# Kernel optimization log

Hardware: AMD Instinct MI355X
Metric: run time of the kernel (lower is better)

The kernel has to match this reference:

```python
import jax, jax.numpy as jnp
import numpy as np

B, S, D = 4, 2048, 1024

def setup_inputs() -> dict:
    key = jax.random.key(0)
    ks = jax.random.split(key, 9)
    q = jax.random.normal(ks[0], (B, S, D), dtype=jnp.float32)
    k = jax.random.normal(ks[1], (B, S, D), dtype=jnp.float32)
    v = jax.random.normal(ks[2], (B, S, D), dtype=jnp.float32)
    # Dense layer params (Glorot-ish scale), bias included like keras Dense
    sc = 1.0 / np.sqrt(D)
    Wq = jax.random.normal(ks[3], (D, D), dtype=jnp.float32) * sc
    Wk = jax.random.normal(ks[4], (D, D), dtype=jnp.float32) * sc
    Wv = jax.random.normal(ks[5], (D, D), dtype=jnp.float32) * sc
    bq = jnp.zeros((D,), dtype=jnp.float32)
    bk = jnp.zeros((D,), dtype=jnp.float32)
    bv = jnp.zeros((D,), dtype=jnp.float32)
    # causal mask: 1 where attention is forbidden (future positions)
    mask = jnp.triu(jnp.ones((S, S), dtype=jnp.float32), k=1)
    return {"q": q, "k": k, "v": v, "mask": mask,
            "Wq": Wq, "bq": bq, "Wk": Wk, "bk": bk, "Wv": Wv, "bv": bv}

def reference(q, k, v, mask, Wq, bq, Wk, bk, Wv, bv):
    WQ = q @ Wq + bq                      # [B,S,D]
    WK = k @ Wk + bk
    WV = v @ Wv + bv
    d_k = jnp.asarray(WK.shape[-1], dtype=jnp.float32)
    scores = jnp.einsum('bqd,bkd->bqk', WQ, WK) / jnp.sqrt(d_k)  # [B,S,S]
    scores = scores + mask * (-1e9)
    attn = jax.nn.softmax(scores, axis=-1)
    return jnp.einsum('bqk,bkd->bqd', attn, WV)
```

## Files before the change

kernel.cpp:

```cpp
#include <hip/hip_runtime.h>
#include <math.h>

#define S_LEN 2048
#define D_DIM 1024
#define NB    4

typedef __bf16 bf16_t;
typedef __bf16 bf16x8 __attribute__((ext_vector_type(8)));
typedef float  f32x4  __attribute__((ext_vector_type(4)));
typedef unsigned int   u32;
typedef unsigned short u16;
typedef unsigned int   u32x4 __attribute__((ext_vector_type(4)));

#define BM 128
#define BN 128
#define BK 64

__device__ __forceinline__ u16 f2b_bits(float x) {
    bf16_t h = (bf16_t)x;
    return *(u16*)&h;
}

__device__ __forceinline__ void async16(const void* g, void* l) {
    __builtin_amdgcn_global_load_lds(
        (__attribute__((address_space(1))) const void*)g,
        (__attribute__((address_space(3))) void*)l, 16, 0, 0);
}

#define BAR_RAW() asm volatile("s_barrier" ::: "memory")

__device__ __forceinline__ void gemm_bt_core(
    const bf16_t* __restrict__ A, const bf16_t* __restrict__ Bt,
    int lda, int ldb, int m0, int n0, int kTiles, f32x4 (&acc)[4][4])
{
    __shared__ bf16_t lA[BM * BK];
    __shared__ bf16_t lB[BN * BK];
    const int t    = threadIdx.x;
    const int w    = t >> 6;
    const int lane = t & 63;
    const int wr   = w >> 1, wc = w & 1;
    const int srow   = lane >> 3;
    const int kb_src = ((lane & 7) ^ (lane >> 3)) * 8;
    const int fr = lane & 15, fq = lane >> 4;
    const int fof0 = (((0 * 4 + fq) ^ (fr & 7)) * 8);
    const int fof1 = (((1 * 4 + fq) ^ (fr & 7)) * 8);
    const bf16_t* paB0 = lA + (wr * 64 + fr) * BK + fof0;
    const bf16_t* paB1 = lA + (wr * 64 + fr) * BK + fof1;
    const bf16_t* pbB0 = lB + (wc * 64 + fr) * BK + fof0;
    const bf16_t* pbB1 = lB + (wc * 64 + fr) * BK + fof1;
    bf16_t* ldsA = lA + (w * 32) * BK;
    bf16_t* ldsB = lB + (w * 32) * BK;
    const bf16_t* gA = A  + (long)(m0 + w * 32 + srow) * lda + kb_src;
    const bf16_t* gB = Bt + (long)(n0 + w * 32 + srow) * ldb + kb_src;

#pragma unroll
    for (int mt = 0; mt < 4; ++mt)
#pragma unroll
        for (int nt = 0; nt < 4; ++nt)
            acc[mt][nt] = f32x4{0.f, 0.f, 0.f, 0.f};

    for (int kt = 0; kt < kTiles; ++kt) {
        const long k0 = (long)kt * BK;
#pragma unroll
        for (int i = 0; i < 4; ++i) {
            async16(gA + k0 + (long)(i * 8) * lda, ldsA + i * 8 * BK);
            async16(gB + k0 + (long)(i * 8) * ldb, ldsB + i * 8 * BK);
        }
        asm volatile("s_waitcnt vmcnt(0)" ::: "memory");
        __syncthreads();
#pragma unroll
        for (int h = 0; h < 2; ++h) {
            const bf16_t* pa = h ? paB1 : paB0;
            const bf16_t* pb = h ? pbB1 : pbB0;
            bf16x8 af[4], bfv[4];
#pragma unroll
            for (int mt = 0; mt < 4; ++mt)
                af[mt] = *(const bf16x8*)(pa + mt * 16 * BK);
#pragma unroll
            for (int nt = 0; nt < 4; ++nt)
                bfv[nt] = *(const bf16x8*)(pb + nt * 16 * BK);
#pragma unroll
            for (int mt = 0; mt < 4; ++mt)
#pragma unroll
                for (int nt = 0; nt < 4; ++nt)
                    acc[mt][nt] = __builtin_amdgcn_mfma_f32_16x16x32_bf16(
                        af[mt], bfv[nt], acc[mt][nt], 0, 0, 0);
        }
        __syncthreads();
    }
}

__device__ __forceinline__ void gemm_bt_dbuf(
    const bf16_t* __restrict__ A, const bf16_t* __restrict__ Bt,
    int lda, int ldb, int m0, int n0, int kTiles, f32x4 (&acc)[4][4])
{
    __shared__ bf16_t lA[2][BM * BK];
    __shared__ bf16_t lB[2][BN * BK];
    const int t    = threadIdx.x;
    const int w    = t >> 6;
    const int lane = t & 63;
    const int wr   = w >> 1, wc = w & 1;
    const int srow   = lane >> 3;
    const int kb_src = ((lane & 7) ^ (lane >> 3)) * 8;
    const int fr = lane & 15, fq = lane >> 4;
    const int fof0 = (((0 * 4 + fq) ^ (fr & 7)) * 8);
    const int fof1 = (((1 * 4 + fq) ^ (fr & 7)) * 8);
    const int aO0 = (wr * 64 + fr) * BK + fof0;
    const int aO1 = (wr * 64 + fr) * BK + fof1;
    const int bO0 = (wc * 64 + fr) * BK + fof0;
    const int bO1 = (wc * 64 + fr) * BK + fof1;
    const int sOf = (w * 32) * BK;
    const bf16_t* gA = A  + (long)(m0 + w * 32 + srow) * lda + kb_src;
    const bf16_t* gB = Bt + (long)(n0 + w * 32 + srow) * ldb + kb_src;

#pragma unroll
    for (int mt = 0; mt < 4; ++mt)
#pragma unroll
        for (int nt = 0; nt < 4; ++nt)
            acc[mt][nt] = f32x4{0.f, 0.f, 0.f, 0.f};

#pragma unroll
    for (int i = 0; i < 4; ++i) {
        async16(gA + (long)(i * 8) * lda, &lA[0][sOf + i * 8 * BK]);
        async16(gB + (long)(i * 8) * ldb, &lB[0][sOf + i * 8 * BK]);
    }

    for (int kt = 0; kt < kTiles; ++kt) {
        const int cur = kt & 1, nxt = cur ^ 1;
        if (kt + 1 < kTiles) {
            const long k1 = (long)(kt + 1) * BK;
#pragma unroll
            for (int i = 0; i < 4; ++i) {
                async16(gA + k1 + (long)(i * 8) * lda, &lA[nxt][sOf + i * 8 * BK]);
                async16(gB + k1 + (long)(i * 8) * ldb, &lB[nxt][sOf + i * 8 * BK]);
            }
            asm volatile("s_waitcnt vmcnt(8)" ::: "memory");
        } else {
            asm volatile("s_waitcnt vmcnt(0)" ::: "memory");
        }
        BAR_RAW();
        const bf16_t* lac = lA[cur];
        const bf16_t* lbc = lB[cur];
#pragma unroll
        for (int h = 0; h < 2; ++h) {
            const bf16_t* pa = lac + (h ? aO1 : aO0);
            const bf16_t* pb = lbc + (h ? bO1 : bO0);
            bf16x8 af[4], bfv[4];
#pragma unroll
            for (int mt = 0; mt < 4; ++mt)
                af[mt] = *(const bf16x8*)(pa + mt * 16 * BK);
#pragma unroll
            for (int nt = 0; nt < 4; ++nt)
                bfv[nt] = *(const bf16x8*)(pb + nt * 16 * BK);
#pragma unroll
            for (int mt = 0; mt < 4; ++mt)
#pragma unroll
                for (int nt = 0; nt < 4; ++nt)
                    acc[mt][nt] = __builtin_amdgcn_mfma_f32_16x16x32_bf16(
                        af[mt], bfv[nt], acc[mt][nt], 0, 0, 0);
        }
        BAR_RAW();
    }
}

__global__ __launch_bounds__(256) void k_f2b(
    const float* __restrict__ q, const float* __restrict__ k,
    const float* __restrict__ v, bf16_t* __restrict__ Xb)
{
    const int z = blockIdx.z;
    const float* src = (z == 0) ? q : ((z == 1) ? k : v);
    bf16_t* dst = Xb + (long)z * ((long)NB * S_LEN * D_DIM);
    const long i = (long)blockIdx.x * blockDim.x + threadIdx.x;
    float4 a = ((const float4*)src)[i];
    u32 lo = (u32)f2b_bits(a.x) | ((u32)f2b_bits(a.y) << 16);
    u32 hi = (u32)f2b_bits(a.z) | ((u32)f2b_bits(a.w) << 16);
    ((uint2*)(dst))[i] = make_uint2(lo, hi);
}

__global__ __launch_bounds__(256) void k_tw(
    const float* __restrict__ Wq, const float* __restrict__ Wk,
    const float* __restrict__ Wv, bf16_t* __restrict__ Wt)
{
    __shared__ u32 tile[64][33];
    const int z = blockIdx.z;
    const float* W = (z == 0) ? Wq : ((z == 1) ? Wk : Wv);
    bf16_t* T = Wt + (long)z * D_DIM * D_DIM;
    const int t = threadIdx.x;
    const int k0 = blockIdx.x * 64, n0 = blockIdx.y * 64;
#pragma unroll
    for (int rr = 0; rr < 4; ++rr) {
        const int kr = (t >> 4) + rr * 16;
        const int nq = (t & 15) * 4;
        float4 f = *(const float4*)(W + (long)(k0 + kr) * D_DIM + n0 + nq);
        tile[kr][(nq >> 1)]     = (u32)f2b_bits(f.x) | ((u32)f2b_bits(f.y) << 16);
        tile[kr][(nq >> 1) + 1] = (u32)f2b_bits(f.z) | ((u32)f2b_bits(f.w) << 16);
    }
    __syncthreads();
#pragma unroll
    for (int rr = 0; rr < 2; ++rr) {
        const int nr = (t >> 3) + rr * 32;
        const int j0 = (t & 7) * 4;
        u32x4 o;
#pragma unroll
        for (int jj = 0; jj < 4; ++jj) {
            const int j = j0 + jj;
            const u32 ua = tile[2 * j][nr >> 1];
            const u32 ub = tile[2 * j + 1][nr >> 1];
            const u32 lo = (nr & 1) ? (ua >> 16) : (ua & 0xffffu);
            const u32 hi = (nr & 1) ? (ub >> 16) : (ub & 0xffffu);
            o[jj] = lo | (hi << 16);
        }
        *(u32x4*)(T + (long)(n0 + nr) * D_DIM + k0 + 2 * j0) = o;
    }
}

__global__ __launch_bounds__(256) void k_tv(
    const bf16_t* __restrict__ PrV, bf16_t* __restrict__ WVt)
{
    __shared__ u32 tile[64][33];
    const int b = blockIdx.z;
    const bf16_t* src = PrV + (long)b * S_LEN * D_DIM;
    bf16_t* dst = WVt + (long)b * D_DIM * S_LEN;
    const int t = threadIdx.x;
    const int d0 = blockIdx.x * 64, s0 = blockIdx.y * 64;
#pragma unroll
    for (int rr = 0; rr < 2; ++rr) {
        const int sr = (t >> 3) + rr * 32;
        const int dp0 = (t & 7) * 4;
        u32x4 u = *(const u32x4*)(src + (long)(s0 + sr) * D_DIM + d0 + 2 * dp0);
#pragma unroll
        for (int q = 0; q < 4; ++q) tile[sr][dp0 + q] = u[q];
    }
    __syncthreads();
#pragma unroll
    for (int rr = 0; rr < 2; ++rr) {
        const int dr = (t >> 3) + rr * 32;
        const int j0 = (t & 7) * 4;
        u32x4 o;
#pragma unroll
        for (int jj = 0; jj < 4; ++jj) {
            const int j = j0 + jj;
            const u32 ua = tile[2 * j][dr >> 1];
            const u32 ub = tile[2 * j + 1][dr >> 1];
            const u32 lo = (dr & 1) ? (ua >> 16) : (ua & 0xffffu);
            const u32 hi = (dr & 1) ? (ub >> 16) : (ub & 0xffffu);
            o[jj] = lo | (hi << 16);
        }
        *(u32x4*)(dst + (long)(d0 + dr) * S_LEN + s0 + 2 * j0) = o;
    }
}

__global__ __launch_bounds__(256) void k_gemm_proj(
    const bf16_t* __restrict__ Xb, const bf16_t* __restrict__ Wt,
    const float* __restrict__ bq, const float* __restrict__ bk,
    const float* __restrict__ bv, bf16_t* __restrict__ Pr)
{
    const int z = blockIdx.z;
    const bf16_t* A  = Xb + (long)z * ((long)NB * S_LEN * D_DIM);
    const bf16_t* Bt = Wt + (long)z * D_DIM * D_DIM;
    bf16_t* C        = Pr + (long)z * ((long)NB * S_LEN * D_DIM);
    const float* bias = (z == 0) ? bq : ((z == 1) ? bk : bv);
    const int m0 = blockIdx.x * BM, n0 = blockIdx.y * BN;
    f32x4 acc[4][4];
    gemm_bt_core(A, Bt, D_DIM, D_DIM, m0, n0, D_DIM / BK, acc);
    const int lane = threadIdx.x & 63, w = threadIdx.x >> 6;
    const int wr = w >> 1, wc = w & 1;
    const int r0 = m0 + wr * 64 + (lane >> 4) * 4;
    const int c0 = n0 + wc * 64 + (lane & 15);
#pragma unroll
    for (int mt = 0; mt < 4; ++mt)
#pragma unroll
        for (int nt = 0; nt < 4; ++nt) {
            const int col = c0 + nt * 16;
            const float bb = bias[col];
#pragma unroll
            for (int r = 0; r < 4; ++r) {
                const int row = r0 + mt * 16 + r;
                C[(long)row * D_DIM + col] = (bf16_t)(acc[mt][nt][r] + bb);
            }
        }
}

__global__ __launch_bounds__(256) void k_gemm_scores(
    const bf16_t* __restrict__ PrQ, const bf16_t* __restrict__ PrK,
    bf16_t* __restrict__ SC)
{
    const int u = blockIdx.x, b = blockIdx.z;
    int ti = (int)((sqrtf(8.0f * (float)u + 1.0f) - 1.0f) * 0.5f);
    while ((ti + 1) * (ti + 2) / 2 <= u) ++ti;
    while (ti * (ti + 1) / 2 > u) --ti;
    const int tj = u - ti * (ti + 1) / 2;
    const bf16_t* A  = PrQ + (long)b * S_LEN * D_DIM;
    const bf16_t* Bt = PrK + (long)b * S_LEN * D_DIM;
    bf16_t* C        = SC  + (long)b * S_LEN * S_LEN;
    const int m0 = ti * BM, n0 = tj * BN;
    f32x4 acc[4][4];
    gemm_bt_dbuf(A, Bt, D_DIM, D_DIM, m0, n0, D_DIM / BK, acc);
    const int lane = threadIdx.x & 63, w = threadIdx.x >> 6;
    const int wr = w >> 1, wc = w & 1;
    const int r0 = m0 + wr * 64 + (lane >> 4) * 4;
    const int c0 = n0 + wc * 64 + (lane & 15);
#pragma unroll
    for (int mt = 0; mt < 4; ++mt)
#pragma unroll
        for (int nt = 0; nt < 4; ++nt) {
            const int col = c0 + nt * 16;
#pragma unroll
            for (int r = 0; r < 4; ++r) {
                const int row = r0 + mt * 16 + r;
                C[(long)row * S_LEN + col] = (bf16_t)(acc[mt][nt][r] * 0.03125f);
            }
        }
}

__global__ __launch_bounds__(256) void k_softmax(bf16_t* __restrict__ SC)
{
    const int w = threadIdx.x >> 6, lane = threadIdx.x & 63;
    const int i = blockIdx.x * 4 + w;
    const int b = blockIdx.y;
    bf16_t* row = SC + ((long)b * S_LEN + i) * S_LEN;
    const int n    = i + 1;
    const int jend = ((i >> 7) + 1) << 7;
    const int nch  = (jend + 511) >> 9;
    float x[4][8];
    float mx = -1e30f;
#pragma unroll
    for (int c = 0; c < 4; ++c) {
        if (c < nch) {
            bf16x8 vv = *(const bf16x8*)(row + c * 512 + lane * 8);
#pragma unroll
            for (int e = 0; e < 8; ++e) {
                const int j = c * 512 + lane * 8 + e;
                const float f = (j < n) ? (float)vv[e] : -1e30f;
                x[c][e] = f;
                mx = fmaxf(mx, f);
            }
        }
    }
#pragma unroll
    for (int d = 1; d < 64; d <<= 1) mx = fmaxf(mx, __shfl_xor(mx, d, 64));
    float sm = 0.f;
#pragma unroll
    for (int c = 0; c < 4; ++c) {
        if (c < nch) {
#pragma unroll
            for (int e = 0; e < 8; ++e) {
                const int j = c * 512 + lane * 8 + e;
                float p = (j < n) ? __expf(x[c][e] - mx) : 0.f;
                x[c][e] = p;
                sm += p;
            }
        }
    }
#pragma unroll
    for (int d = 1; d < 64; d <<= 1) sm += __shfl_xor(sm, d, 64);
    const float inv = 1.0f / sm;
#pragma unroll
    for (int c = 0; c < 4; ++c) {
        if (c < nch) {
            bf16x8 o;
#pragma unroll
            for (int e = 0; e < 8; ++e) o[e] = (bf16_t)(x[c][e] * inv);
            *(bf16x8*)(row + c * 512 + lane * 8) = o;
        }
    }
}

__global__ __launch_bounds__(256) void k_gemm_pv(
    const bf16_t* __restrict__ SC, const bf16_t* __restrict__ WVt,
    float* __restrict__ Out)
{
    const int ti = (S_LEN / BM - 1) - blockIdx.y, b = blockIdx.z;
    const bf16_t* A  = SC  + (long)b * S_LEN * S_LEN;
    const bf16_t* Bt = WVt + (long)b * D_DIM * S_LEN;
    float* C         = Out + (long)b * S_LEN * D_DIM;
    const int m0 = ti * BM, n0 = blockIdx.x * BN;
    f32x4 acc[4][4];
    gemm_bt_dbuf(A, Bt, S_LEN, S_LEN, m0, n0, (ti + 1) * (BM / BK), acc);
    const int lane = threadIdx.x & 63, w = threadIdx.x >> 6;
    const int wr = w >> 1, wc = w & 1;
    const int r0 = m0 + wr * 64 + (lane >> 4) * 4;
    const int c0 = n0 + wc * 64 + (lane & 15);
#pragma unroll
    for (int mt = 0; mt < 4; ++mt)
#pragma unroll
        for (int nt = 0; nt < 4; ++nt) {
            const int col = c0 + nt * 16;
#pragma unroll
            for (int r = 0; r < 4; ++r) {
                const int row = r0 + mt * 16 + r;
                C[(long)row * D_DIM + col] = acc[mt][nt][r];
            }
        }
}

extern "C" void kernel_launch(void* const* d_in, const int* in_sizes, int n_in,
                              void* d_out, int out_size, void* d_ws, size_t ws_size,
                              hipStream_t stream)
{
    (void)in_sizes; (void)n_in; (void)out_size; (void)ws_size;
    const float* q  = (const float*)d_in[0];
    const float* k  = (const float*)d_in[1];
    const float* v  = (const float*)d_in[2];
    const float* Wq = (const float*)d_in[4];
    const float* bq = (const float*)d_in[5];
    const float* Wk = (const float*)d_in[6];
    const float* bk = (const float*)d_in[7];
    const float* Wv = (const float*)d_in[8];
    const float* bv = (const float*)d_in[9];
    float* out = (float*)d_out;

    bf16_t* ws = (bf16_t*)d_ws;
    const long nW = (long)D_DIM * D_DIM;
    const long nX = (long)NB * S_LEN * D_DIM;
    bf16_t* Wt  = ws;
    bf16_t* Xb  = Wt + 3 * nW;
    bf16_t* SC  = Xb;
    bf16_t* Pr  = Xb + 3 * nX;
    bf16_t* WVt = Pr + 3 * nX;
    bf16_t* PrQ = Pr;
    bf16_t* PrK = Pr + nX;
    bf16_t* PrV = Pr + 2 * nX;

    k_f2b        <<<dim3(8192, 1, 3),   256,        0, stream>>>(q, k, v, Xb);
    k_tw         <<<dim3(16, 16, 3),    256,        0, stream>>>(Wq, Wk, Wv, Wt);
    k_gemm_proj  <<<dim3(64, 8, 3),     256,        0, stream>>>(Xb, Wt, bq, bk, bv, Pr);
    k_tv         <<<dim3(16, 32, NB),   256,        0, stream>>>(PrV, WVt);
    k_gemm_scores<<<dim3(136, 1, NB),   256,        0, stream>>>(PrQ, PrK, SC);
    k_softmax    <<<dim3(S_LEN / 4, NB),256,        0, stream>>>(SC);
    k_gemm_pv    <<<dim3(8, 16, NB),    256,        0, stream>>>(SC, WVt, out);
}
```

Measured before the change: 316.1 us.

## Replace projection GEMM with 256x256 eight-wave double-buffered interleaved-load kernel

Replaces the single-buffered 128x128 projection GEMM with a 512-thread, 256x256-tile kernel. It double-buffers LDS and issues global-to-LDS async loads for the next K tiles between four MFMA phases, and raises wave priority during MFMA bursts. The larger tile improves data reuse per load, and the interleaving is meant to hide global load latency behind compute. In exchange it needs more registers and LDS per block, and launches fewer blocks (384), which may limit occupancy or load balance.

```diff
diff --git a/kernel.cpp b/kernel.cpp
--- a/kernel.cpp
+++ b/kernel.cpp
@@ -15,6 +15,8 @@
 #define BM 128
 #define BN 128
 #define BK 64
+#define BM2 256
+#define BN2 256
 
 __device__ __forceinline__ u16 f2b_bits(float x) {
     bf16_t h = (bf16_t)x;
@@ -29,73 +31,187 @@
 
 #define BAR_RAW() asm volatile("s_barrier" ::: "memory")
 
-__device__ __forceinline__ void gemm_bt_core(
-    const bf16_t* __restrict__ A, const bf16_t* __restrict__ Bt,
-    int lda, int ldb, int m0, int n0, int kTiles, f32x4 (&acc)[4][4])
-{
-    __shared__ bf16_t lA[BM * BK];
-    __shared__ bf16_t lB[BN * BK];
-    const int t    = threadIdx.x;
-    const int w    = t >> 6;
-    const int lane = t & 63;
-    const int wr   = w >> 1, wc = w & 1;
-    const int srow   = lane >> 3;
-    const int kb_src = ((lane & 7) ^ (lane >> 3)) * 8;
+__global__ __launch_bounds__(512, 2) void k_gemm_proj8(
+    const bf16_t* __restrict__ Xb, const bf16_t* __restrict__ Wt,
+    const float* __restrict__ bq, const float* __restrict__ bk,
+    const float* __restrict__ bv, bf16_t* __restrict__ Pr)
+{
+    __shared__ __attribute__((aligned(16))) bf16_t lA[2][BM2 * BK];
+    __shared__ __attribute__((aligned(16))) bf16_t lB[2][BN2 * BK];
+    const int z = blockIdx.z;
+    const bf16_t* A  = Xb + (long)z * ((long)NB * S_LEN * D_DIM);
+    const bf16_t* Bt = Wt + (long)z * D_DIM * D_DIM;
+    bf16_t* C        = Pr + (long)z * ((long)NB * S_LEN * D_DIM);
+    const float* bias = (z == 0) ? bq : ((z == 1) ? bk : bv);
+    const int m0 = blockIdx.x * BM2, n0 = blockIdx.y * BN2;
+    const int KT = D_DIM / BK;
+
+    const int t = threadIdx.x;
+    const int w = t >> 6, lane = t & 63;
+    const int wr = w >> 2, wc = w & 3;
+    const int srow = lane >> 3, slot = lane & 7;
+    const int kb_src = (slot ^ srow) * 8;
     const int fr = lane & 15, fq = lane >> 4;
-    const int fof0 = (((0 * 4 + fq) ^ (fr & 7)) * 8);
-    const int fof1 = (((1 * 4 + fq) ^ (fr & 7)) * 8);
-    const bf16_t* paB0 = lA + (wr * 64 + fr) * BK + fof0;
-    const bf16_t* paB1 = lA + (wr * 64 + fr) * BK + fof1;
-    const bf16_t* pbB0 = lB + (wc * 64 + fr) * BK + fof0;
-    const bf16_t* pbB1 = lB + (wc * 64 + fr) * BK + fof1;
-    bf16_t* ldsA = lA + (w * 32) * BK;
-    bf16_t* ldsB = lB + (w * 32) * BK;
-    const bf16_t* gA = A  + (long)(m0 + w * 32 + srow) * lda + kb_src;
-    const bf16_t* gB = Bt + (long)(n0 + w * 32 + srow) * ldb + kb_src;
-
-#pragma unroll
-    for (int mt = 0; mt < 4; ++mt)
+    const int fofh0 = ((fq       ^ (fr & 7)) * 8);
+    const int fofh1 = (((4 + fq) ^ (fr & 7)) * 8);
+    const int rbA = (wr * 128 + fr) * BK;
+    const int rbB = (wc * 64  + fr) * BK;
+
+    const bf16_t* gA = A  + (long)(m0 + w * 8 + srow) * D_DIM + kb_src;
+    const bf16_t* gB = Bt + (long)(n0 + w * 8 + srow) * D_DIM + kb_src;
+    const int ldsw = (w * 8) * BK;
+
+    f32x4 acc[8][4];
+#pragma unroll
+    for (int mt = 0; mt < 8; ++mt)
 #pragma unroll
         for (int nt = 0; nt < 4; ++nt)
             acc[mt][nt] = f32x4{0.f, 0.f, 0.f, 0.f};
 
-    for (int kt = 0; kt < kTiles; ++kt) {
-        const long k0 = (long)kt * BK;
-#pragma unroll
-        for (int i = 0; i < 4; ++i) {
-            async16(gA + k0 + (long)(i * 8) * lda, ldsA + i * 8 * BK);
-            async16(gB + k0 + (long)(i * 8) * ldb, ldsB + i * 8 * BK);
-        }
-        asm volatile("s_waitcnt vmcnt(0)" ::: "memory");
-        __syncthreads();
-#pragma unroll
-        for (int h = 0; h < 2; ++h) {
-            const bf16_t* pa = h ? paB1 : paB0;
-            const bf16_t* pb = h ? pbB1 : pbB0;
-            bf16x8 af[4], bfv[4];
-#pragma unroll
-            for (int mt = 0; mt < 4; ++mt)
-                af[mt] = *(const bf16x8*)(pa + mt * 16 * BK);
-#pragma unroll
-            for (int nt = 0; nt < 4; ++nt)
-                bfv[nt] = *(const bf16x8*)(pb + nt * 16 * BK);
-#pragma unroll
-            for (int mt = 0; mt < 4; ++mt)
-#pragma unroll
-                for (int nt = 0; nt < 4; ++nt)
-                    acc[mt][nt] = __builtin_amdgcn_mfma_f32_16x16x32_bf16(
-                        af[mt], bfv[nt], acc[mt][nt], 0, 0, 0);
-        }
-        __syncthreads();
-    }
+    {
+        const long kc1 = BK;
+        async16(gA,                     &lA[0][0   * BK + ldsw]);
+        async16(gA + (long)64  * D_DIM, &lA[0][64  * BK + ldsw]);
+        async16(gA + (long)128 * D_DIM, &lA[0][128 * BK + ldsw]);
+        async16(gA + (long)192 * D_DIM, &lA[0][192 * BK + ldsw]);
+        async16(gB,                     &lB[0][0   * BK + ldsw]);
+        async16(gB + (long)64  * D_DIM, &lB[0][64  * BK + ldsw]);
+        async16(gB + (long)128 * D_DIM, &lB[0][128 * BK + ldsw]);
+        async16(gB + (long)192 * D_DIM, &lB[0][192 * BK + ldsw]);
+        async16(gA + kc1,                     &lA[1][0   * BK + ldsw]);
+        async16(gA + kc1 + (long)64  * D_DIM, &lA[1][64  * BK + ldsw]);
+        async16(gA + kc1 + (long)128 * D_DIM, &lA[1][128 * BK + ldsw]);
+        async16(gA + kc1 + (long)192 * D_DIM, &lA[1][192 * BK + ldsw]);
+        asm volatile("s_waitcnt vmcnt(4)" ::: "memory");
+        BAR_RAW();
+    }
+
+#pragma unroll 1
+    for (int J = 0; J < KT; ++J) {
+        const int pb = J & 1;
+        const bf16_t* lab = lA[pb];
+        const bf16_t* lbb = lB[pb];
+        bf16_t* lbn = lB[pb ^ 1];
+        bf16_t* laS = lA[pb];
+        const long kc1 = (long)(J + 1) * BK;
+        const long kc2 = (long)(J + 2) * BK;
+        bf16x8 af[4][2], b0f[2][2], b1f[2][2];
+
+#pragma unroll
+        for (int mt = 0; mt < 4; ++mt) {
+            af[mt][0] = *(const bf16x8*)(lab + rbA + mt * 16 * BK + fofh0);
+            af[mt][1] = *(const bf16x8*)(lab + rbA + mt * 16 * BK + fofh1);
+        }
+#pragma unroll
+        for (int nt = 0; nt < 2; ++nt) {
+            b0f[nt][0] = *(const bf16x8*)(lbb + rbB + nt * 16 * BK + fofh0);
+            b0f[nt][1] = *(const bf16x8*)(lbb + rbB + nt * 16 * BK + fofh1);
+        }
+        if (J + 1 < KT) {
+            async16(gB + kc1,                    lbn + 0  * BK + ldsw);
+            async16(gB + kc1 + (long)64 * D_DIM, lbn + 64 * BK + ldsw);
+        }
+        BAR_RAW();
+        __builtin_amdgcn_s_setprio(1);
+#pragma unroll
+        for (int mt = 0; mt < 4; ++mt)
+#pragma unroll
+            for (int nt = 0; nt < 2; ++nt) {
+                acc[mt][nt] = __builtin_amdgcn_mfma_f32_16x16x32_bf16(
+                    af[mt][0], b0f[nt][0], acc[mt][nt], 0, 0, 0);
+                acc[mt][nt] = __builtin_amdgcn_mfma_f32_16x16x32_bf16(
+                    af[mt][1], b0f[nt][1], acc[mt][nt], 0, 0, 0);
+            }
+        __builtin_amdgcn_s_setprio(0);
+        BAR_RAW();
+
+#pragma unroll
+        for (int nt = 0; nt < 2; ++nt) {
+            b1f[nt][0] = *(const bf16x8*)(lbb + rbB + (2 + nt) * 16 * BK + fofh0);
+            b1f[nt][1] = *(const bf16x8*)(lbb + rbB + (2 + nt) * 16 * BK + fofh1);
+        }
+        if (J + 1 < KT) {
+            async16(gB + kc1 + (long)128 * D_DIM, lbn + 128 * BK + ldsw);
+            async16(gB + kc1 + (long)192 * D_DIM, lbn + 192 * BK + ldsw);
+        }
+        BAR_RAW();
+        __builtin_amdgcn_s_setprio(1);
+#pragma unroll
+        for (int mt = 0; mt < 4; ++mt)
+#pragma unroll
+            for (int nt = 0; nt < 2; ++nt) {
+                acc[mt][2 + nt] = __builtin_amdgcn_mfma_f32_16x16x32_bf16(
+                    af[mt][0], b1f[nt][0], acc[mt][2 + nt], 0, 0, 0);
+                acc[mt][2 + nt] = __builtin_amdgcn_mfma_f32_16x16x32_bf16(
+                    af[mt][1], b1f[nt][1], acc[mt][2 + nt], 0, 0, 0);
+            }
+        __builtin_amdgcn_s_setprio(0);
+        BAR_RAW();
+
+#pragma unroll
+        for (int mt = 0; mt < 4; ++mt) {
+            af[mt][0] = *(const bf16x8*)(lab + rbA + (64 + mt * 16) * BK + fofh0);
+            af[mt][1] = *(const bf16x8*)(lab + rbA + (64 + mt * 16) * BK + fofh1);
+        }
+        BAR_RAW();
+        __builtin_amdgcn_s_setprio(1);
+#pragma unroll
+        for (int mt = 0; mt < 4; ++mt)
+#pragma unroll
+            for (int nt = 0; nt < 2; ++nt) {
+                acc[4 + mt][2 + nt] = __builtin_amdgcn_mfma_f32_16x16x32_bf16(
+                    af[mt][0], b1f[nt][0], acc[4 + mt][2 + nt], 0, 0, 0);
+                acc[4 + mt][2 + nt] = __builtin_amdgcn_mfma_f32_16x16x32_bf16(
+                    af[mt][1], b1f[nt][1], acc[4 + mt][2 + nt], 0, 0, 0);
+            }
+        __builtin_amdgcn_s_setprio(0);
+        BAR_RAW();
+
+        if (J + 2 < KT) {
+            async16(gA + kc2,                     laS + 0   * BK + ldsw);
+            async16(gA + kc2 + (long)64  * D_DIM, laS + 64  * BK + ldsw);
+            async16(gA + kc2 + (long)128 * D_DIM, laS + 128 * BK + ldsw);
+            async16(gA + kc2 + (long)192 * D_DIM, laS + 192 * BK + ldsw);
+        }
+        BAR_RAW();
+        __builtin_amdgcn_s_setprio(1);
+#pragma unroll
+        for (int mt = 0; mt < 4; ++mt)
+#pragma unroll
+            for (int nt = 0; nt < 2; ++nt) {
+                acc[4 + mt][nt] = __builtin_amdgcn_mfma_f32_16x16x32_bf16(
+                    af[mt][0], b0f[nt][0], acc[4 + mt][nt], 0, 0, 0);
+                acc[4 + mt][nt] = __builtin_amdgcn_mfma_f32_16x16x32_bf16(
+                    af[mt][1], b0f[nt][1], acc[4 + mt][nt], 0, 0, 0);
+            }
+        __builtin_amdgcn_s_setprio(0);
+        if (J + 2 < KT)      asm volatile("s_waitcnt vmcnt(4)" ::: "memory");
+        else if (J + 1 < KT) asm volatile("s_waitcnt vmcnt(0)" ::: "memory");
+        BAR_RAW();
+    }
+
+    const int r0 = m0 + wr * 128 + fq * 4;
+    const int c0 = n0 + wc * 64 + fr;
+#pragma unroll
+    for (int mt = 0; mt < 8; ++mt)
+#pragma unroll
+        for (int nt = 0; nt < 4; ++nt) {
+            const int col = c0 + nt * 16;
+            const float bb = bias[col];
+#pragma unroll
+            for (int r = 0; r < 4; ++r) {
+                const int row = r0 + mt * 16 + r;
+                C[(long)row * D_DIM + col] = (bf16_t)(acc[mt][nt][r] + bb);
+            }
+        }
 }
 
 __device__ __forceinline__ void gemm_bt_dbuf(
     const bf16_t* __restrict__ A, const bf16_t* __restrict__ Bt,
     int lda, int ldb, int m0, int n0, int kTiles, f32x4 (&acc)[4][4])
 {
-    __shared__ bf16_t lA[2][BM * BK];
-    __shared__ bf16_t lB[2][BN * BK];
+    __shared__ __attribute__((aligned(16))) bf16_t lA[2][BM * BK];
+    __shared__ __attribute__((aligned(16))) bf16_t lB[2][BN * BK];
     const int t    = threadIdx.x;
     const int w    = t >> 6;
     const int lane = t & 63;
@@ -250,37 +366,6 @@
     }
 }
 
-__global__ __launch_bounds__(256) void k_gemm_proj(
-    const bf16_t* __restrict__ Xb, const bf16_t* __restrict__ Wt,
-    const float* __restrict__ bq, const float* __restrict__ bk,
-    const float* __restrict__ bv, bf16_t* __restrict__ Pr)
-{
-    const int z = blockIdx.z;
-    const bf16_t* A  = Xb + (long)z * ((long)NB * S_LEN * D_DIM);
-    const bf16_t* Bt = Wt + (long)z * D_DIM * D_DIM;
-    bf16_t* C        = Pr + (long)z * ((long)NB * S_LEN * D_DIM);
-    const float* bias = (z == 0) ? bq : ((z == 1) ? bk : bv);
-    const int m0 = blockIdx.x * BM, n0 = blockIdx.y * BN;
-    f32x4 acc[4][4];
-    gemm_bt_core(A, Bt, D_DIM, D_DIM, m0, n0, D_DIM / BK, acc);
-    const int lane = threadIdx.x & 63, w = threadIdx.x >> 6;
-    const int wr = w >> 1, wc = w & 1;
-    const int r0 = m0 + wr * 64 + (lane >> 4) * 4;
-    const int c0 = n0 + wc * 64 + (lane & 15);
-#pragma unroll
-    for (int mt = 0; mt < 4; ++mt)
-#pragma unroll
-        for (int nt = 0; nt < 4; ++nt) {
-            const int col = c0 + nt * 16;
-            const float bb = bias[col];
-#pragma unroll
-            for (int r = 0; r < 4; ++r) {
-                const int row = r0 + mt * 16 + r;
-                C[(long)row * D_DIM + col] = (bf16_t)(acc[mt][nt][r] + bb);
-            }
-        }
-}
-
 __global__ __launch_bounds__(256) void k_gemm_scores(
     const bf16_t* __restrict__ PrQ, const bf16_t* __restrict__ PrK,
     bf16_t* __restrict__ SC)
@@ -424,7 +509,7 @@
 
     k_f2b        <<<dim3(8192, 1, 3),   256,        0, stream>>>(q, k, v, Xb);
     k_tw         <<<dim3(16, 16, 3),    256,        0, stream>>>(Wq, Wk, Wv, Wt);
-    k_gemm_proj  <<<dim3(64, 8, 3),     256,        0, stream>>>(Xb, Wt, bq, bk, bv, Pr);
+    k_gemm_proj8 <<<dim3(32, 4, 3),     512,        0, stream>>>(Xb, Wt, bq, bk, bv, Pr);
     k_tv         <<<dim3(16, 32, NB),   256,        0, stream>>>(PrV, WVt);
     k_gemm_scores<<<dim3(136, 1, NB),   256,        0, stream>>>(PrQ, PrK, SC);
     k_softmax    <<<dim3(S_LEN / 4, NB),256,        0, stream>>>(SC);
```

Result: slower. 331.2 us (+4.8%).
